# Optimization experiments

Hardware: AMD Instinct MI355X
Metric: run time of the kernel (lower is better)

## Reference

```python
import jax, jax.numpy as jnp
import numpy as np

NHEAD = 3
NPTS = 5
HID = 96
B_GRAPHS = 16384
COORDS_WEIGHT = 1.0


def _ln(x, g, b):
    mu = jnp.mean(x, -1, keepdims=True)
    v = jnp.mean((x - mu) ** 2, -1, keepdims=True)
    return (x - mu) / jnp.sqrt(v + 1e-5) * g + b


def _build_edge_index():
    # fully-connected per graph, grouped by source node (row-major over sources)
    idx = np.arange(NPTS)
    src = np.repeat(idx, NPTS - 1)
    dst = np.concatenate([np.delete(idx, i) for i in range(NPTS)])
    off = (np.arange(B_GRAPHS) * NPTS)[:, None]
    row = (off + src[None, :]).reshape(-1)
    col = (off + dst[None, :]).reshape(-1)
    return jnp.asarray(np.stack([row, col]), dtype=jnp.int32)


def setup_inputs():
    key = jax.random.key(0)
    ks = jax.random.split(key, 24)
    Nn = B_GRAPHS * NPTS          # 81920 nodes
    E = B_GRAPHS * NPTS * (NPTS - 1)  # 327680 edges

    def w(k, i, o):
        return jax.random.normal(k, (i, o), jnp.float32) * (1.0 / np.sqrt(i))

    inp = {
        'h': jax.random.normal(ks[0], (Nn, HID), jnp.float32),
        'edge_index': _build_edge_index(),
        'coord': jax.random.normal(ks[1], (Nn, 3), jnp.float32),
        'coord_pre': jax.random.normal(ks[2], (Nn, 3), jnp.float32),
        'vel': jax.random.normal(ks[3], (Nn, 3), jnp.float32),
        'edge_attr': jax.random.normal(ks[4], (E, HID), jnp.float32),
        # edge_mlp
        'ew1': w(ks[5], 3 * HID, HID), 'eb1': jnp.zeros((HID,), jnp.float32),
        'ew2': w(ks[6], HID, HID), 'eb2': jnp.zeros((HID,), jnp.float32),
        # edge_mlp_enhance
        'xw1': w(ks[7], 3 * HID, HID), 'xb1': jnp.zeros((HID,), jnp.float32),
        'xw2': w(ks[8], HID, HID), 'xb2': jnp.zeros((HID,), jnp.float32),
        # node_mlp
        'nw1': w(ks[9], 2 * HID, HID), 'nb1': jnp.zeros((HID,), jnp.float32),
        'nw2': w(ks[10], HID, HID), 'nb2': jnp.zeros((HID,), jnp.float32),
        # coord_mlp_inner
        'cw1': w(ks[11], HID, HID), 'cb1': jnp.zeros((HID,), jnp.float32),
        'cw2': w(ks[12], HID, HID), 'cb2': jnp.zeros((HID,), jnp.float32),
        'cw3': w(ks[13], HID, 3), 'cb3': jnp.zeros((3,), jnp.float32),
        # attention projections
        'qw': w(ks[14], HID, HID), 'qb': jnp.zeros((HID,), jnp.float32),
        'kw': w(ks[15], 2 * HID, HID), 'kb': jnp.zeros((HID,), jnp.float32),
        'vw': w(ks[16], HID, HID), 'vb': jnp.zeros((HID,), jnp.float32),
        # layernorms
        'g1': jnp.ones((HID,), jnp.float32), 'be1': jnp.zeros((HID,), jnp.float32),
        'g2': jnp.ones((HID,), jnp.float32), 'be2': jnp.zeros((HID,), jnp.float32),
    }
    return inp


def _forward(h, edge_index, coord, coord_pre, vel, edge_attr,
             ew1, eb1, ew2, eb2, xw1, xb1, xw2, xb2, nw1, nb1, nw2, nb2,
             cw1, cb1, cw2, cb2, cw3, cb3, qw, qb, kw, kb, vw, vb,
             g1, be1, g2, be2):
    sp = jax.nn.softplus
    row, col = edge_index[0], edge_index[1]
    n_nodes = h.shape[0]

    # edge_model (attention flag is False)
    ef = sp(jnp.concatenate([h[row], h[col], edge_attr], 1) @ ew1 + eb1)
    ef = sp(ef @ ew2 + eb2)  # [E, C]

    B, N, C = n_nodes // NPTS, NPTS, ef.shape[-1]
    d = C // NHEAD
    q = h.reshape(B, N, C)
    m = ef.reshape(B, N, N - 1, C)
    h_m = jnp.concatenate(
        [jnp.broadcast_to(q[:, :, None, :], (B, N, N - 1, C)), m], -1
    ).reshape(B, N * (N - 1), 2 * C)

    qh = (q @ qw + qb).reshape(B, N, NHEAD, d).transpose(0, 2, 1, 3)           # [B,H,N,d]
    kh = (h_m @ kw + kb).reshape(B, N * (N - 1), NHEAD, d).transpose(0, 2, 1, 3)
    kh = kh.reshape(B, NHEAD, N, N - 1, d)                                      # [B,H,N,N-1,d]
    vh = (ef.reshape(B, N * (N - 1), C) @ vw + vb).reshape(B, N * (N - 1), NHEAD, d).transpose(0, 2, 1, 3)

    scores = jnp.einsum('bhnd,bhnkd->bhnk', qh, kh) / jnp.sqrt(jnp.float32(d))
    attw = jax.nn.softmax(scores, -1)                                           # [B,H,N,N-1]
    m_update = attw.reshape(B, NHEAD, N * (N - 1), 1) * vh                      # [B,H,E',d]
    att_edge_feat = m_update.transpose(0, 2, 1, 3).reshape(-1, C)               # [E, C]

    # node_model
    agg = jax.ops.segment_sum(att_edge_feat, row, num_segments=n_nodes)
    agg = _ln(agg, g1, be1)
    out = sp(jnp.concatenate([h, agg], 1) @ nw1 + nb1) @ nw2 + nb2
    hn = _ln(h + out, g2, be2)

    # edge enhance
    ef2 = ef + (sp(jnp.concatenate([hn[row], hn[col], edge_attr], 1) @ xw1 + xb1) @ xw2 + xb2)

    # coord2radial on coord_pre (norm_diff=False)
    cd = coord_pre[row] - coord_pre[col]
    cc = jnp.cross(coord_pre[row], coord_pre[col])
    cv = jnp.cross(cd, cc)

    # acc_model_inner
    t = sp(ef2 @ cw1 + cb1)
    t = sp(t @ cw2 + cb2)
    bc = t @ cw3 + cb3                                                          # [E, 3]
    trans = jnp.clip(cd * bc[:, :1] + cc * bc[:, 1:2] + cv * bc[:, 2:3], -100.0, 100.0)
    s = jax.ops.segment_sum(trans, row, num_segments=n_nodes)
    cnt = jax.ops.segment_sum(jnp.ones_like(trans), row, num_segments=n_nodes)
    acc = (s / jnp.maximum(cnt, 1.0)) * COORDS_WEIGHT

    return acc, hn, ef2


def reference(h, edge_index, coord, coord_pre, vel, edge_attr,
              ew1, eb1, ew2, eb2, xw1, xb1, xw2, xb2, nw1, nb1, nw2, nb2,
              cw1, cb1, cw2, cb2, cw3, cb3, qw, qb, kw, kb, vw, vb,
              g1, be1, g2, be2):
    return _forward(h, edge_index, coord, coord_pre, vel, edge_attr,
                    ew1, eb1, ew2, eb2, xw1, xb1, xw2, xb2, nw1, nb1, nw2, nb2,
                    cw1, cb1, cw2, cb2, cw3, cb3, qw, qb, kw, kb, vw, vb,
                    g1, be1, g2, be2)
```

## Files before the change

kernel.cpp:

```cpp
#include <hip/hip_runtime.h>
#include <hip/hip_bf16.h>

#define B_GRAPHS 16384
#define NN (B_GRAPHS * 5)
#define NE (NN * 4)
#define GPB 4
#define EPB 80
#define NPB 20

typedef __attribute__((ext_vector_type(8))) short bf8;
typedef __attribute__((ext_vector_type(4))) short s4;
typedef __attribute__((ext_vector_type(4))) float f4;
typedef __attribute__((ext_vector_type(2))) unsigned u2;
typedef __attribute__((ext_vector_type(4))) unsigned u4;

#define OFF_EW1 0
#define OFF_EW2 27648
#define OFF_KW  36864
#define OFF_VW  55296
#define OFF_QW  64512
#define OFF_NW1 73728
#define OFF_NW2 92160
#define OFF_XW1 101376
#define OFF_XW2 129024
#define OFF_CW1 138240
#define OFF_CW2 147456

__device__ __forceinline__ float sp_f(float x) {
    return fmaxf(x, 0.0f) + __logf(1.0f + __expf(-fabsf(x)));
}
__device__ __forceinline__ short tobf(float x) {
    return __builtin_bit_cast(short, __float2bfloat16(x));
}
__device__ __forceinline__ float frombf(short s) {
    union { float f; unsigned u; } v;
    v.u = ((unsigned)(unsigned short)s) << 16;
    return v.f;
}
__device__ __forceinline__ unsigned pk2(float a, float b) {
    unsigned lo = (unsigned short)tobf(a);
    unsigned hi = (unsigned short)tobf(b);
    return lo | (hi << 16);
}
__device__ __forceinline__ bf8 ldfrag(const short* buf, int row, int k) {
    return *(const bf8*)&buf[(row * 96 + k) ^ ((row & 7) << 3)];
}
__device__ __forceinline__ void stpk(short* buf, int row, int col0, f4 v) {
    u2 o = {pk2(v[0], v[1]), pk2(v[2], v[3])};
    *(u2*)&buf[(row * 96 + col0) ^ ((row & 7) << 3)] = o;
}
__device__ __forceinline__ void stpk8(short* buf, int row, int col0,
                                      const float* v) {
    u4 o = {pk2(v[0], v[1]), pk2(v[2], v[3]), pk2(v[4], v[5]), pk2(v[6], v[7])};
    *(u4*)&buf[(row * 96 + col0) ^ ((row & 7) << 3)] = o;
}
__device__ __forceinline__ float* oaddr(float* b, int row, int col) {
    return &b[(row * 96 + col) ^ ((row & 7) << 2)];
}

template <int K, int NS, class AF>
__device__ __forceinline__ void gemmCol(const short* __restrict__ wT, int wc0,
                                        int ln, int kg, AF aload, f4* acc) {
#pragma unroll
    for (int s = 0; s < NS; s++) {
        acc[s][0] = 0.f; acc[s][1] = 0.f; acc[s][2] = 0.f; acc[s][3] = 0.f;
    }
#pragma unroll
    for (int k0 = 0; k0 < K; k0 += 32) {
        bf8 wf = *(const bf8*)(wT + (size_t)(wc0 + ln) * K + k0 + kg * 8);
#pragma unroll
        for (int s = 0; s < NS; s++) {
            acc[s] = __builtin_amdgcn_mfma_f32_16x16x32_bf16(wf, aload(s, k0),
                                                             acc[s], 0, 0, 0);
        }
    }
}

__global__ __launch_bounds__(256) void k_prep(
    const float* ew1, const float* ew2, const float* kw, const float* vw,
    const float* qw, const float* nw1, const float* nw2, const float* xw1,
    const float* xw2, const float* cw1, const float* cw2, short* wsT) {
    const float* srcs[11] = {ew1, ew2, kw, vw, qw, nw1, nw2, xw1, xw2, cw1, cw2};
    const int Ks[11] = {288, 96, 192, 96, 96, 192, 96, 288, 96, 96, 96};
    const int offs[11] = {OFF_EW1, OFF_EW2, OFF_KW, OFF_VW, OFF_QW, OFF_NW1,
                          OFF_NW2, OFF_XW1, OFF_XW2, OFF_CW1, OFF_CW2};
    int b = blockIdx.x;
    const float* src = srcs[b];
    int K = Ks[b], off = offs[b];
    for (int idx = threadIdx.x; idx < K * 96; idx += 256) {
        int n = idx / K, k = idx - n * K;
        wsT[off + idx] = tobf(src[(size_t)k * 96 + n]);
    }
}

__global__ __launch_bounds__(384, 4) void k_fused(
    const float* __restrict__ h, const float* __restrict__ cp,
    const float* __restrict__ ea, const short* __restrict__ wsT,
    const float* __restrict__ eb1, const float* __restrict__ eb2,
    const float* __restrict__ qb, const float* __restrict__ kb,
    const float* __restrict__ vb, const float* __restrict__ nb1,
    const float* __restrict__ nb2, const float* __restrict__ g1,
    const float* __restrict__ be1, const float* __restrict__ g2,
    const float* __restrict__ be2, const float* __restrict__ xb1,
    const float* __restrict__ xb2, const float* __restrict__ cb1,
    const float* __restrict__ cb2, const float* __restrict__ cw3,
    const float* __restrict__ cb3,
    float* __restrict__ accg, float* __restrict__ hng, float* __restrict__ efg) {
    __shared__ __align__(16) short smem[24960];
    short* hb  = smem;
    short* S1  = smem + 1920;
    short* efb = smem + 9600;
    short* kvb = smem + 17280;
    short* qag = S1 + 48 * 96;
    float* sc   = (float*)S1;
    float* outb = (float*)(S1 + 3072);
    float* cw3e = (float*)efb;
    float* bcb  = (float*)(efb + 576);
    float* trs  = (float*)(efb + 1056);

    const int t = threadIdx.x;
    const int blk = blockIdx.x;
    const int n0 = blk * NPB, e0 = blk * EPB;

    for (int i = t; i < 1920; i += 384) {
        int r = i / 24, c = (i - r * 24) * 4;
        f4 v = *(const f4*)&ea[(size_t)(e0 + r) * 96 + c];
        stpk(kvb, r, c, v);
    }
    for (int i = t; i < 480; i += 384) {
        int r = i / 24, c = (i - r * 24) * 4;
        f4 v = *(const f4*)&h[(size_t)(n0 + r) * 96 + c];
        stpk(hb, r, c, v);
    }
    __syncthreads();

    const int lane = t & 63, w = t >> 6;
    const int kg = lane >> 4, ln = lane & 15;
    const int wc0 = w * 16, col0 = wc0 + kg * 4;

    int erow[5], esrc[5], edst[5];
#pragma unroll
    for (int s = 0; s < 5; s++) {
        erow[s] = s * 16 + ln;
        int sl = erow[s] >> 2;
        esrc[s] = sl;
        int si = sl % 5, jj = erow[s] & 3;
        edst[s] = (sl / 5) * 5 + jj + (jj >= si);
    }

    f4 acc[5];
    gemmCol<288, 5>(wsT + OFF_EW1, wc0, ln, kg,
        [&](int s, int k0) -> bf8 {
            int k = k0 + kg * 8;
            if (k0 < 96)  return ldfrag(hb, esrc[s], k);
            if (k0 < 192) return ldfrag(hb, edst[s], k - 96);
            return ldfrag(kvb, erow[s], k - 192);
        }, acc);
    {
        f4 b = *(const f4*)&eb1[col0];
#pragma unroll
        for (int s = 0; s < 5; s++) {
            f4 v;
#pragma unroll
            for (int j = 0; j < 4; j++) v[j] = sp_f(acc[s][j] + b[j]);
            stpk(S1, erow[s], col0, v);
        }
    }
    __syncthreads();
    gemmCol<96, 5>(wsT + OFF_EW2, wc0, ln, kg,
        [&](int s, int k0) { return ldfrag(S1, erow[s], k0 + kg * 8); }, acc);
    {
        f4 b = *(const f4*)&eb2[col0];
#pragma unroll
        for (int s = 0; s < 5; s++) {
            f4 v;
#pragma unroll
            for (int j = 0; j < 4; j++) v[j] = sp_f(acc[s][j] + b[j]);
            stpk(efb, erow[s], col0, v);
        }
    }
    __syncthreads();
    {
        f4 qa[2];
        gemmCol<96, 2>(wsT + OFF_QW, wc0, ln, kg,
            [&](int s, int k0) { return ldfrag(hb, s * 16 + ln, k0 + kg * 8); }, qa);
        f4 b = *(const f4*)&qb[col0];
#pragma unroll
        for (int s = 0; s < 2; s++) {
            int row = s * 16 + ln;
            if (row < NPB) {
                f4 v;
#pragma unroll
                for (int j = 0; j < 4; j++) v[j] = qa[s][j] + b[j];
                stpk(qag, row, col0, v);
            }
        }
    }
    gemmCol<192, 5>(wsT + OFF_KW, wc0, ln, kg,
        [&](int s, int k0) {
            int k = k0 + kg * 8;
            if (k0 < 96) return ldfrag(hb, esrc[s], k);
            return ldfrag(efb, erow[s], k - 96);
        }, acc);
    {
        f4 b = *(const f4*)&kb[col0];
#pragma unroll
        for (int s = 0; s < 5; s++) {
            f4 v;
#pragma unroll
            for (int j = 0; j < 4; j++) v[j] = acc[s][j] + b[j];
            stpk(kvb, erow[s], col0, v);
        }
    }
    __syncthreads();
    if (t < 240) {
        int e = t / 3, hd = t - e * 3, nd = e >> 2;
        float s = 0.f;
#pragma unroll
        for (int c8 = 0; c8 < 4; c8++) {
            int c = hd * 32 + c8 * 8;
            bf8 qv = ldfrag(qag, nd, c);
            bf8 kv = ldfrag(kvb, e, c);
#pragma unroll
            for (int j = 0; j < 8; j++) s = fmaf(frombf(qv[j]), frombf(kv[j]), s);
        }
        sc[e * 3 + hd] = s * 0.17677669529663687f;
    }
    __syncthreads();
    if (t < 60) {
        int nd = t / 3, hd = t - nd * 3;
        float v0 = sc[(nd * 4 + 0) * 3 + hd], v1 = sc[(nd * 4 + 1) * 3 + hd];
        float v2 = sc[(nd * 4 + 2) * 3 + hd], v3 = sc[(nd * 4 + 3) * 3 + hd];
        float m = fmaxf(fmaxf(v0, v1), fmaxf(v2, v3));
        float p0 = __expf(v0 - m), p1 = __expf(v1 - m);
        float p2 = __expf(v2 - m), p3 = __expf(v3 - m);
        float inv = 1.f / (p0 + p1 + p2 + p3);
        sc[(nd * 4 + 0) * 3 + hd] = p0 * inv;
        sc[(nd * 4 + 1) * 3 + hd] = p1 * inv;
        sc[(nd * 4 + 2) * 3 + hd] = p2 * inv;
        sc[(nd * 4 + 3) * 3 + hd] = p3 * inv;
    }
    gemmCol<96, 5>(wsT + OFF_VW, wc0, ln, kg,
        [&](int s, int k0) { return ldfrag(efb, erow[s], k0 + kg * 8); }, acc);
    {
        f4 b = *(const f4*)&vb[col0];
#pragma unroll
        for (int s = 0; s < 5; s++) {
            f4 v;
#pragma unroll
            for (int j = 0; j < 4; j++) v[j] = acc[s][j] + b[j];
            stpk(kvb, erow[s], col0, v);
        }
    }
    __syncthreads();
    if (t < 320) {
        int nd = t >> 4, cg = t & 15;
        bool act = cg < 12;
        int hd = cg >> 2;
        float agg[8];
#pragma unroll
        for (int j = 0; j < 8; j++) agg[j] = 0.f;
        if (act) {
#pragma unroll
            for (int k = 0; k < 4; k++) {
                int e = nd * 4 + k;
                float wgt = sc[e * 3 + hd];
                bf8 v8 = ldfrag(kvb, e, cg * 8);
#pragma unroll
                for (int j = 0; j < 8; j++) agg[j] = fmaf(wgt, frombf(v8[j]), agg[j]);
            }
        }
        float s1 = 0.f, s2 = 0.f;
#pragma unroll
        for (int j = 0; j < 8; j++) { s1 += agg[j]; s2 += agg[j] * agg[j]; }
        if (!act) { s1 = 0.f; s2 = 0.f; }
        for (int m = 1; m < 16; m <<= 1) {
            s1 += __shfl_xor(s1, m);
            s2 += __shfl_xor(s2, m);
        }
        float mu = s1 * (1.f / 96.f);
        float var = s2 * (1.f / 96.f) - mu * mu;
        float rs = rsqrtf(var + 1e-5f);
        if (act) {
            int c = cg * 8;
            f4 ga = *(const f4*)&g1[c], gb = *(const f4*)&g1[c + 4];
            f4 ba = *(const f4*)&be1[c], bb = *(const f4*)&be1[c + 4];
            float o[8];
#pragma unroll
            for (int j = 0; j < 4; j++) {
                o[j] = (agg[j] - mu) * rs * ga[j] + ba[j];
                o[j + 4] = (agg[j + 4] - mu) * rs * gb[j] + bb[j];
            }
            stpk8(qag, nd, c, o);
        }
    }
    __syncthreads();
    for (int i = t; i < 1920; i += 384) {
        int r = i / 24, c = (i - r * 24) * 4;
        f4 v = *(const f4*)&ea[(size_t)(e0 + r) * 96 + c];
        stpk(kvb, r, c, v);
    }
    {
        f4 na[2];
        gemmCol<192, 2>(wsT + OFF_NW1, wc0, ln, kg,
            [&](int s, int k0) {
                int row = s * 16 + ln, k = k0 + kg * 8;
                if (k0 < 96) return ldfrag(hb, row, k);
                return ldfrag(qag, row, k - 96);
            }, na);
        f4 b = *(const f4*)&nb1[col0];
#pragma unroll
        for (int s = 0; s < 2; s++) {
            int row = s * 16 + ln;
            f4 v;
#pragma unroll
            for (int j = 0; j < 4; j++) v[j] = sp_f(na[s][j] + b[j]);
            stpk(S1, row, col0, v);
        }
    }
    __syncthreads();
    {
        f4 na[2];
        gemmCol<96, 2>(wsT + OFF_NW2, wc0, ln, kg,
            [&](int s, int k0) { return ldfrag(S1, s * 16 + ln, k0 + kg * 8); }, na);
        f4 b = *(const f4*)&nb2[col0];
#pragma unroll
        for (int s = 0; s < 2; s++) {
            int row = s * 16 + ln;
            if (row < NPB) {
                f4 hv = *(const f4*)&h[(size_t)(n0 + row) * 96 + col0];
                f4 v;
#pragma unroll
                for (int j = 0; j < 4; j++) v[j] = na[s][j] + b[j] + hv[j];
                *(f4*)oaddr(outb, row, col0) = v;
            }
        }
    }
    __syncthreads();
    if (t < 320) {
        int nd = t >> 4, cg = t & 15;
        bool act = cg < 12;
        float xv[8];
#pragma unroll
        for (int j = 0; j < 8; j++) xv[j] = 0.f;
        if (act) {
            f4 x0 = *(const f4*)oaddr(outb, nd, cg * 8);
            f4 x1 = *(const f4*)oaddr(outb, nd, cg * 8 + 4);
#pragma unroll
            for (int j = 0; j < 4; j++) { xv[j] = x0[j]; xv[j + 4] = x1[j]; }
        }
        float s1 = 0.f, s2 = 0.f;
#pragma unroll
        for (int j = 0; j < 8; j++) { s1 += xv[j]; s2 += xv[j] * xv[j]; }
        for (int m = 1; m < 16; m <<= 1) {
            s1 += __shfl_xor(s1, m);
            s2 += __shfl_xor(s2, m);
        }
        float mu = s1 * (1.f / 96.f);
        float var = s2 * (1.f / 96.f) - mu * mu;
        float rs = rsqrtf(var + 1e-5f);
        if (act) {
            int c = cg * 8;
            f4 ga = *(const f4*)&g2[c], gb = *(const f4*)&g2[c + 4];
            f4 ba = *(const f4*)&be2[c], bb = *(const f4*)&be2[c + 4];
            float o[8];
#pragma unroll
            for (int j = 0; j < 4; j++) {
                o[j] = (xv[j] - mu) * rs * ga[j] + ba[j];
                o[j + 4] = (xv[j + 4] - mu) * rs * gb[j] + bb[j];
            }
            f4 o0 = {o[0], o[1], o[2], o[3]}, o1 = {o[4], o[5], o[6], o[7]};
            *(f4*)&hng[(size_t)(n0 + nd) * 96 + c] = o0;
            *(f4*)&hng[(size_t)(n0 + nd) * 96 + c + 4] = o1;
            stpk8(hb, nd, c, o);
        }
    }
    __syncthreads();
    gemmCol<288, 5>(wsT + OFF_XW1, wc0, ln, kg,
        [&](int s, int k0) -> bf8 {
            int k = k0 + kg * 8;
            if (k0 < 96)  return ldfrag(hb, esrc[s], k);
            if (k0 < 192) return ldfrag(hb, edst[s], k - 96);
            return ldfrag(kvb, erow[s], k - 192);
        }, acc);
    {
        f4 b = *(const f4*)&xb1[col0];
#pragma unroll
        for (int s = 0; s < 5; s++) {
            f4 v;
#pragma unroll
            for (int j = 0; j < 4; j++) v[j] = sp_f(acc[s][j] + b[j]);
            stpk(S1, erow[s], col0, v);
        }
    }
    __syncthreads();
    gemmCol<96, 5>(wsT + OFF_XW2, wc0, ln, kg,
        [&](int s, int k0) { return ldfrag(S1, erow[s], k0 + kg * 8); }, acc);
    {
        f4 b = *(const f4*)&xb2[col0];
#pragma unroll
        for (int s = 0; s < 5; s++) {
            int row = erow[s];
            s4 ev = *(const s4*)&efb[(row * 96 + col0) ^ ((row & 7) << 3)];
            f4 v;
#pragma unroll
            for (int j = 0; j < 4; j++) v[j] = acc[s][j] + b[j] + frombf(ev[j]);
            *(f4*)&efg[(size_t)(e0 + row) * 96 + col0] = v;
            stpk(efb, row, col0, v);
        }
    }
    __syncthreads();
    gemmCol<96, 5>(wsT + OFF_CW1, wc0, ln, kg,
        [&](int s, int k0) { return ldfrag(efb, erow[s], k0 + kg * 8); }, acc);
    {
        f4 b = *(const f4*)&cb1[col0];
#pragma unroll
        for (int s = 0; s < 5; s++) {
            f4 v;
#pragma unroll
            for (int j = 0; j < 4; j++) v[j] = sp_f(acc[s][j] + b[j]);
            stpk(S1, erow[s], col0, v);
        }
    }
    __syncthreads();
    if (t < 288) cw3e[t] = cw3[t];
    gemmCol<96, 5>(wsT + OFF_CW2, wc0, ln, kg,
        [&](int s, int k0) { return ldfrag(S1, erow[s], k0 + kg * 8); }, acc);
    {
        f4 b = *(const f4*)&cb2[col0];
#pragma unroll
        for (int s = 0; s < 5; s++) {
            f4 v;
#pragma unroll
            for (int j = 0; j < 4; j++) v[j] = sp_f(acc[s][j] + b[j]);
            stpk(kvb, erow[s], col0, v);
        }
    }
    __syncthreads();
    if (t < 240) {
        int e = t / 3, j = t - e * 3;
        float s = cb3[j];
#pragma unroll
        for (int c8 = 0; c8 < 12; c8++) {
            bf8 av = ldfrag(kvb, e, c8 * 8);
#pragma unroll
            for (int jj = 0; jj < 8; jj++)
                s = fmaf(frombf(av[jj]), cw3e[(c8 * 8 + jj) * 3 + j], s);
        }
        bcb[e * 3 + j] = s;
    }
    __syncthreads();
    if (t < 80) {
        int sl = t >> 2, jj = t & 3, si = sl % 5;
        int dl = (sl / 5) * 5 + jj + (jj >= si);
        int rn = n0 + sl, cn = n0 + dl;
        float r0c = cp[(size_t)rn * 3 + 0], r1c = cp[(size_t)rn * 3 + 1],
              r2c = cp[(size_t)rn * 3 + 2];
        float q0 = cp[(size_t)cn * 3 + 0], q1 = cp[(size_t)cn * 3 + 1],
              q2 = cp[(size_t)cn * 3 + 2];
        float d0 = r0c - q0, d1 = r1c - q1, d2 = r2c - q2;
        float x0 = r1c * q2 - r2c * q1;
        float x1 = r2c * q0 - r0c * q2;
        float x2 = r0c * q1 - r1c * q0;
        float v0 = d1 * x2 - d2 * x1;
        float v1 = d2 * x0 - d0 * x2;
        float v2 = d0 * x1 - d1 * x0;
        float b0 = bcb[t * 3 + 0], b1 = bcb[t * 3 + 1], b2 = bcb[t * 3 + 2];
        trs[t * 4 + 0] = fminf(fmaxf(d0 * b0 + x0 * b1 + v0 * b2, -100.f), 100.f);
        trs[t * 4 + 1] = fminf(fmaxf(d1 * b0 + x1 * b1 + v1 * b2, -100.f), 100.f);
        trs[t * 4 + 2] = fminf(fmaxf(d2 * b0 + x2 * b1 + v2 * b2, -100.f), 100.f);
    }
    __syncthreads();
    if (t < 60) {
        int nd = t / 3, j = t - nd * 3;
        float s = (trs[(nd * 4 + 0) * 4 + j] + trs[(nd * 4 + 1) * 4 + j] +
                   trs[(nd * 4 + 2) * 4 + j] + trs[(nd * 4 + 3) * 4 + j]) * 0.25f;
        accg[(size_t)(n0 + nd) * 3 + j] = s;
    }
}

extern "C" void kernel_launch(void* const* d_in, const int* in_sizes, int n_in,
                              void* d_out, int out_size, void* d_ws, size_t ws_size,
                              hipStream_t stream) {
    const float* h   = (const float*)d_in[0];
    const float* cp  = (const float*)d_in[3];
    const float* ea  = (const float*)d_in[5];
    const float* ew1 = (const float*)d_in[6];
    const float* eb1 = (const float*)d_in[7];
    const float* ew2 = (const float*)d_in[8];
    const float* eb2 = (const float*)d_in[9];
    const float* xw1 = (const float*)d_in[10];
    const float* xb1 = (const float*)d_in[11];
    const float* xw2 = (const float*)d_in[12];
    const float* xb2 = (const float*)d_in[13];
    const float* nw1 = (const float*)d_in[14];
    const float* nb1 = (const float*)d_in[15];
    const float* nw2 = (const float*)d_in[16];
    const float* nb2 = (const float*)d_in[17];
    const float* cw1 = (const float*)d_in[18];
    const float* cb1 = (const float*)d_in[19];
    const float* cw2 = (const float*)d_in[20];
    const float* cb2 = (const float*)d_in[21];
    const float* cw3 = (const float*)d_in[22];
    const float* cb3 = (const float*)d_in[23];
    const float* qw  = (const float*)d_in[24];
    const float* qb  = (const float*)d_in[25];
    const float* kw  = (const float*)d_in[26];
    const float* kb  = (const float*)d_in[27];
    const float* vw  = (const float*)d_in[28];
    const float* vb  = (const float*)d_in[29];
    const float* g1  = (const float*)d_in[30];
    const float* be1 = (const float*)d_in[31];
    const float* g2  = (const float*)d_in[32];
    const float* be2 = (const float*)d_in[33];

    float* out  = (float*)d_out;
    float* accg = out;
    float* hng  = out + (size_t)NN * 3;
    float* efg  = out + (size_t)NN * 3 + (size_t)NN * 96;
    short* wsT = (short*)d_ws;

    k_prep<<<11, 256, 0, stream>>>(ew1, ew2, kw, vw, qw, nw1, nw2, xw1, xw2,
                                   cw1, cw2, wsT);
    k_fused<<<B_GRAPHS / GPB, 384, 0, stream>>>(
        h, cp, ea, wsT, eb1, eb2, qb, kb, vb, nb1, nb2, g1, be1, g2, be2,
        xb1, xb2, cb1, cb2, cw3, cb3, accg, hng, efg);
}
```

Before: 355.8 us.

## Replace XOR-swizzled LDS layout with padded rows and restructure buffer reuse

Switches shared-memory tiles from an XOR swizzle on a 96-wide row to a padded 104-element row stride, using precomputed row base offsets to avoid conflicts with simpler address math. Buffers are reassigned so the edge-MLP second layer overlaps the Q projection with one fewer barrier. The edge-attribute reload is issued into registers before the node-MLP GEMM so its latency overlaps compute. Weight fragments are preloaded up front in each GEMM. The node-output buffer now holds bf16 instead of fp32, which changes LayerNorm input precision. More registers and an extra barrier before XW1's epilogue may reduce occupancy.

```diff
diff --git a/kernel.cpp b/kernel.cpp
--- a/kernel.cpp
+++ b/kernel.cpp
@@ -7,6 +7,7 @@
 #define GPB 4
 #define EPB 80
 #define NPB 20
+#define RS 104
 
 typedef __attribute__((ext_vector_type(8))) short bf8;
 typedef __attribute__((ext_vector_type(4))) short s4;
@@ -42,35 +43,36 @@
     unsigned hi = (unsigned short)tobf(b);
     return lo | (hi << 16);
 }
-__device__ __forceinline__ bf8 ldfrag(const short* buf, int row, int k) {
-    return *(const bf8*)&buf[(row * 96 + k) ^ ((row & 7) << 3)];
-}
-__device__ __forceinline__ void stpk(short* buf, int row, int col0, f4 v) {
+__device__ __forceinline__ bf8 ldL(const short* buf, int off) {
+    return *(const bf8*)&buf[off];
+}
+__device__ __forceinline__ void stL(short* buf, int off, f4 v) {
     u2 o = {pk2(v[0], v[1]), pk2(v[2], v[3])};
-    *(u2*)&buf[(row * 96 + col0) ^ ((row & 7) << 3)] = o;
-}
-__device__ __forceinline__ void stpk8(short* buf, int row, int col0,
-                                      const float* v) {
+    *(u2*)&buf[off] = o;
+}
+__device__ __forceinline__ void stL8(short* buf, int off, const float* v) {
     u4 o = {pk2(v[0], v[1]), pk2(v[2], v[3]), pk2(v[4], v[5]), pk2(v[6], v[7])};
-    *(u4*)&buf[(row * 96 + col0) ^ ((row & 7) << 3)] = o;
-}
-__device__ __forceinline__ float* oaddr(float* b, int row, int col) {
-    return &b[(row * 96 + col) ^ ((row & 7) << 2)];
+    *(u4*)&buf[off] = o;
 }
 
 template <int K, int NS, class AF>
 __device__ __forceinline__ void gemmCol(const short* __restrict__ wT, int wc0,
                                         int ln, int kg, AF aload, f4* acc) {
+    constexpr int NK = K / 32;
+    bf8 wf[NK];
+    const short* wp = wT + (size_t)(wc0 + ln) * K + kg * 8;
+#pragma unroll
+    for (int kk = 0; kk < NK; kk++) wf[kk] = *(const bf8*)(wp + kk * 32);
 #pragma unroll
     for (int s = 0; s < NS; s++) {
         acc[s][0] = 0.f; acc[s][1] = 0.f; acc[s][2] = 0.f; acc[s][3] = 0.f;
     }
 #pragma unroll
-    for (int k0 = 0; k0 < K; k0 += 32) {
-        bf8 wf = *(const bf8*)(wT + (size_t)(wc0 + ln) * K + k0 + kg * 8);
+    for (int kk = 0; kk < NK; kk++) {
 #pragma unroll
         for (int s = 0; s < NS; s++) {
-            acc[s] = __builtin_amdgcn_mfma_f32_16x16x32_bf16(wf, aload(s, k0),
+            acc[s] = __builtin_amdgcn_mfma_f32_16x16x32_bf16(wf[kk],
+                                                             aload(s, kk * 32),
                                                              acc[s], 0, 0, 0);
         }
     }
@@ -106,17 +108,15 @@
     const float* __restrict__ cb2, const float* __restrict__ cw3,
     const float* __restrict__ cb3,
     float* __restrict__ accg, float* __restrict__ hng, float* __restrict__ efg) {
-    __shared__ __align__(16) short smem[24960];
-    short* hb  = smem;
-    short* S1  = smem + 1920;
-    short* efb = smem + 9600;
-    short* kvb = smem + 17280;
-    short* qag = S1 + 48 * 96;
-    float* sc   = (float*)S1;
-    float* outb = (float*)(S1 + 3072);
-    float* cw3e = (float*)efb;
-    float* bcb  = (float*)(efb + 576);
-    float* trs  = (float*)(efb + 1056);
+    __shared__ __align__(16) short smem[220 * RS];
+    short* hb = smem;
+    short* SB = smem + 20 * RS;
+    short* E1 = smem + 60 * RS;
+    short* E2 = smem + 140 * RS;
+    float* sc   = (float*)(SB + 20 * RS);
+    float* cw3s = (float*)(SB + 20 * RS);
+    float* bcb  = (float*)(SB + 26 * RS);
+    float* trs  = (float*)(SB + 31 * RS);
 
     const int t = threadIdx.x;
     const int blk = blockIdx.x;
@@ -125,12 +125,12 @@
     for (int i = t; i < 1920; i += 384) {
         int r = i / 24, c = (i - r * 24) * 4;
         f4 v = *(const f4*)&ea[(size_t)(e0 + r) * 96 + c];
-        stpk(kvb, r, c, v);
+        stL(E2, r * RS + c, v);
     }
     for (int i = t; i < 480; i += 384) {
         int r = i / 24, c = (i - r * 24) * 4;
         f4 v = *(const f4*)&h[(size_t)(n0 + r) * 96 + c];
-        stpk(hb, r, c, v);
+        stL(hb, r * RS + c, v);
     }
     __syncthreads();
 
@@ -138,23 +138,25 @@
     const int kg = lane >> 4, ln = lane & 15;
     const int wc0 = w * 16, col0 = wc0 + kg * 4;
 
-    int erow[5], esrc[5], edst[5];
+    int erow[5], ebase[5], sbase[5], dbase[5];
 #pragma unroll
     for (int s = 0; s < 5; s++) {
         erow[s] = s * 16 + ln;
         int sl = erow[s] >> 2;
-        esrc[s] = sl;
         int si = sl % 5, jj = erow[s] & 3;
-        edst[s] = (sl / 5) * 5 + jj + (jj >= si);
+        int dl = (sl / 5) * 5 + jj + (jj >= si);
+        ebase[s] = erow[s] * RS;
+        sbase[s] = sl * RS;
+        dbase[s] = dl * RS;
     }
 
     f4 acc[5];
     gemmCol<288, 5>(wsT + OFF_EW1, wc0, ln, kg,
         [&](int s, int k0) -> bf8 {
             int k = k0 + kg * 8;
-            if (k0 < 96)  return ldfrag(hb, esrc[s], k);
-            if (k0 < 192) return ldfrag(hb, edst[s], k - 96);
-            return ldfrag(kvb, erow[s], k - 192);
+            if (k0 < 96)  return ldL(hb, sbase[s] + k);
+            if (k0 < 192) return ldL(hb, dbase[s] + k - 96);
+            return ldL(E2, ebase[s] + k - 192);
         }, acc);
     {
         f4 b = *(const f4*)&eb1[col0];
@@ -163,44 +165,43 @@
             f4 v;
 #pragma unroll
             for (int j = 0; j < 4; j++) v[j] = sp_f(acc[s][j] + b[j]);
-            stpk(S1, erow[s], col0, v);
+            stL(E1, ebase[s] + col0, v);
         }
     }
     __syncthreads();
     gemmCol<96, 5>(wsT + OFF_EW2, wc0, ln, kg,
-        [&](int s, int k0) { return ldfrag(S1, erow[s], k0 + kg * 8); }, acc);
-    {
-        f4 b = *(const f4*)&eb2[col0];
-#pragma unroll
-        for (int s = 0; s < 5; s++) {
-            f4 v;
-#pragma unroll
-            for (int j = 0; j < 4; j++) v[j] = sp_f(acc[s][j] + b[j]);
-            stpk(efb, erow[s], col0, v);
-        }
-    }
-    __syncthreads();
+        [&](int s, int k0) { return ldL(E1, ebase[s] + k0 + kg * 8); }, acc);
     {
         f4 qa[2];
         gemmCol<96, 2>(wsT + OFF_QW, wc0, ln, kg,
-            [&](int s, int k0) { return ldfrag(hb, s * 16 + ln, k0 + kg * 8); }, qa);
-        f4 b = *(const f4*)&qb[col0];
+            [&](int s, int k0) { return ldL(hb, (s * 16 + ln) * RS + k0 + kg * 8); },
+            qa);
+        f4 b = *(const f4*)&eb2[col0];
+#pragma unroll
+        for (int s = 0; s < 5; s++) {
+            f4 v;
+#pragma unroll
+            for (int j = 0; j < 4; j++) v[j] = sp_f(acc[s][j] + b[j]);
+            stL(E2, ebase[s] + col0, v);
+        }
+        f4 bq = *(const f4*)&qb[col0];
 #pragma unroll
         for (int s = 0; s < 2; s++) {
             int row = s * 16 + ln;
             if (row < NPB) {
                 f4 v;
 #pragma unroll
-                for (int j = 0; j < 4; j++) v[j] = qa[s][j] + b[j];
-                stpk(qag, row, col0, v);
+                for (int j = 0; j < 4; j++) v[j] = qa[s][j] + bq[j];
+                stL(SB, row * RS + col0, v);
             }
         }
     }
+    __syncthreads();
     gemmCol<192, 5>(wsT + OFF_KW, wc0, ln, kg,
         [&](int s, int k0) {
             int k = k0 + kg * 8;
-            if (k0 < 96) return ldfrag(hb, esrc[s], k);
-            return ldfrag(efb, erow[s], k - 96);
+            if (k0 < 96) return ldL(hb, sbase[s] + k);
+            return ldL(E2, ebase[s] + k - 96);
         }, acc);
     {
         f4 b = *(const f4*)&kb[col0];
@@ -209,7 +210,7 @@
             f4 v;
 #pragma unroll
             for (int j = 0; j < 4; j++) v[j] = acc[s][j] + b[j];
-            stpk(kvb, erow[s], col0, v);
+            stL(E1, ebase[s] + col0, v);
         }
     }
     __syncthreads();
@@ -219,8 +220,8 @@
 #pragma unroll
         for (int c8 = 0; c8 < 4; c8++) {
             int c = hd * 32 + c8 * 8;
-            bf8 qv = ldfrag(qag, nd, c);
-            bf8 kv = ldfrag(kvb, e, c);
+            bf8 qv = ldL(SB, nd * RS + c);
+            bf8 kv = ldL(E1, e * RS + c);
 #pragma unroll
             for (int j = 0; j < 8; j++) s = fmaf(frombf(qv[j]), frombf(kv[j]), s);
         }
@@ -241,7 +242,7 @@
         sc[(nd * 4 + 3) * 3 + hd] = p3 * inv;
     }
     gemmCol<96, 5>(wsT + OFF_VW, wc0, ln, kg,
-        [&](int s, int k0) { return ldfrag(efb, erow[s], k0 + kg * 8); }, acc);
+        [&](int s, int k0) { return ldL(E2, ebase[s] + k0 + kg * 8); }, acc);
     {
         f4 b = *(const f4*)&vb[col0];
 #pragma unroll
@@ -249,7 +250,7 @@
             f4 v;
 #pragma unroll
             for (int j = 0; j < 4; j++) v[j] = acc[s][j] + b[j];
-            stpk(kvb, erow[s], col0, v);
+            stL(E1, ebase[s] + col0, v);
         }
     }
     __syncthreads();
@@ -265,7 +266,7 @@
             for (int k = 0; k < 4; k++) {
                 int e = nd * 4 + k;
                 float wgt = sc[e * 3 + hd];
-                bf8 v8 = ldfrag(kvb, e, cg * 8);
+                bf8 v8 = ldL(E1, e * RS + cg * 8);
 #pragma unroll
                 for (int j = 0; j < 8; j++) agg[j] = fmaf(wgt, frombf(v8[j]), agg[j]);
             }
@@ -291,38 +292,47 @@
                 o[j] = (agg[j] - mu) * rs * ga[j] + ba[j];
                 o[j + 4] = (agg[j + 4] - mu) * rs * gb[j] + bb[j];
             }
-            stpk8(qag, nd, c, o);
-        }
-    }
-    __syncthreads();
-    for (int i = t; i < 1920; i += 384) {
-        int r = i / 24, c = (i - r * 24) * 4;
-        f4 v = *(const f4*)&ea[(size_t)(e0 + r) * 96 + c];
-        stpk(kvb, r, c, v);
-    }
-    {
+            stL8(SB, nd * RS + c, o);
+        }
+    }
+    __syncthreads();
+    {
+        f4 eav[5];
+        int rr[5], cc[5];
+#pragma unroll
+        for (int u = 0; u < 5; u++) {
+            int i = t + u * 384;
+            rr[u] = i / 24; cc[u] = (i - rr[u] * 24) * 4;
+            eav[u] = *(const f4*)&ea[(size_t)(e0 + rr[u]) * 96 + cc[u]];
+        }
         f4 na[2];
         gemmCol<192, 2>(wsT + OFF_NW1, wc0, ln, kg,
             [&](int s, int k0) {
                 int row = s * 16 + ln, k = k0 + kg * 8;
-                if (k0 < 96) return ldfrag(hb, row, k);
-                return ldfrag(qag, row, k - 96);
+                if (k0 < 96) return ldL(hb, row * RS + k);
+                return ldL(SB, row * RS + k - 96);
             }, na);
         f4 b = *(const f4*)&nb1[col0];
 #pragma unroll
         for (int s = 0; s < 2; s++) {
             int row = s * 16 + ln;
-            f4 v;
-#pragma unroll
-            for (int j = 0; j < 4; j++) v[j] = sp_f(na[s][j] + b[j]);
-            stpk(S1, row, col0, v);
-        }
+            if (row < NPB) {
+                f4 v;
+#pragma unroll
+                for (int j = 0; j < 4; j++) v[j] = sp_f(na[s][j] + b[j]);
+                stL(SB, (20 + row) * RS + col0, v);
+            }
+        }
+#pragma unroll
+        for (int u = 0; u < 5; u++) stL(E1, rr[u] * RS + cc[u], eav[u]);
     }
     __syncthreads();
     {
         f4 na[2];
         gemmCol<96, 2>(wsT + OFF_NW2, wc0, ln, kg,
-            [&](int s, int k0) { return ldfrag(S1, s * 16 + ln, k0 + kg * 8); }, na);
+            [&](int s, int k0) {
+                return ldL(SB, (20 + s * 16 + ln) * RS + k0 + kg * 8);
+            }, na);
         f4 b = *(const f4*)&nb2[col0];
 #pragma unroll
         for (int s = 0; s < 2; s++) {
@@ -332,7 +342,7 @@
                 f4 v;
 #pragma unroll
                 for (int j = 0; j < 4; j++) v[j] = na[s][j] + b[j] + hv[j];
-                *(f4*)oaddr(outb, row, col0) = v;
+                stL(SB, row * RS + col0, v);
             }
         }
     }
@@ -344,10 +354,9 @@
 #pragma unroll
         for (int j = 0; j < 8; j++) xv[j] = 0.f;
         if (act) {
-            f4 x0 = *(const f4*)oaddr(outb, nd, cg * 8);
-            f4 x1 = *(const f4*)oaddr(outb, nd, cg * 8 + 4);
-#pragma unroll
-            for (int j = 0; j < 4; j++) { xv[j] = x0[j]; xv[j + 4] = x1[j]; }
+            bf8 x = ldL(SB, nd * RS + cg * 8);
+#pragma unroll
+            for (int j = 0; j < 8; j++) xv[j] = frombf(x[j]);
         }
         float s1 = 0.f, s2 = 0.f;
 #pragma unroll
@@ -372,17 +381,18 @@
             f4 o0 = {o[0], o[1], o[2], o[3]}, o1 = {o[4], o[5], o[6], o[7]};
             *(f4*)&hng[(size_t)(n0 + nd) * 96 + c] = o0;
             *(f4*)&hng[(size_t)(n0 + nd) * 96 + c + 4] = o1;
-            stpk8(hb, nd, c, o);
+            stL8(hb, nd * RS + c, o);
         }
     }
     __syncthreads();
     gemmCol<288, 5>(wsT + OFF_XW1, wc0, ln, kg,
         [&](int s, int k0) -> bf8 {
             int k = k0 + kg * 8;
-            if (k0 < 96)  return ldfrag(hb, esrc[s], k);
-            if (k0 < 192) return ldfrag(hb, edst[s], k - 96);
-            return ldfrag(kvb, erow[s], k - 192);
+            if (k0 < 96)  return ldL(hb, sbase[s] + k);
+            if (k0 < 192) return ldL(hb, dbase[s] + k - 96);
+            return ldL(E1, ebase[s] + k - 192);
         }, acc);
+    __syncthreads();
     {
         f4 b = *(const f4*)&xb1[col0];
 #pragma unroll
@@ -390,28 +400,27 @@
             f4 v;
 #pragma unroll
             for (int j = 0; j < 4; j++) v[j] = sp_f(acc[s][j] + b[j]);
-            stpk(S1, erow[s], col0, v);
+            stL(E1, ebase[s] + col0, v);
         }
     }
     __syncthreads();
     gemmCol<96, 5>(wsT + OFF_XW2, wc0, ln, kg,
-        [&](int s, int k0) { return ldfrag(S1, erow[s], k0 + kg * 8); }, acc);
+        [&](int s, int k0) { return ldL(E1, ebase[s] + k0 + kg * 8); }, acc);
     {
         f4 b = *(const f4*)&xb2[col0];
 #pragma unroll
         for (int s = 0; s < 5; s++) {
-            int row = erow[s];
-            s4 ev = *(const s4*)&efb[(row * 96 + col0) ^ ((row & 7) << 3)];
+            s4 ev = *(const s4*)&E2[ebase[s] + col0];
             f4 v;
 #pragma unroll
             for (int j = 0; j < 4; j++) v[j] = acc[s][j] + b[j] + frombf(ev[j]);
-            *(f4*)&efg[(size_t)(e0 + row) * 96 + col0] = v;
-            stpk(efb, row, col0, v);
+            *(f4*)&efg[(size_t)(e0 + erow[s]) * 96 + col0] = v;
+            stL(E2, ebase[s] + col0, v);
         }
     }
     __syncthreads();
     gemmCol<96, 5>(wsT + OFF_CW1, wc0, ln, kg,
-        [&](int s, int k0) { return ldfrag(efb, erow[s], k0 + kg * 8); }, acc);
+        [&](int s, int k0) { return ldL(E2, ebase[s] + k0 + kg * 8); }, acc);
     {
         f4 b = *(const f4*)&cb1[col0];
 #pragma unroll
@@ -419,13 +428,13 @@
             f4 v;
 #pragma unroll
             for (int j = 0; j < 4; j++) v[j] = sp_f(acc[s][j] + b[j]);
-            stpk(S1, erow[s], col0, v);
-        }
-    }
-    __syncthreads();
-    if (t < 288) cw3e[t] = cw3[t];
+            stL(E1, ebase[s] + col0, v);
+        }
+    }
+    __syncthreads();
+    if (t < 288) cw3s[t] = cw3[t];
     gemmCol<96, 5>(wsT + OFF_CW2, wc0, ln, kg,
-        [&](int s, int k0) { return ldfrag(S1, erow[s], k0 + kg * 8); }, acc);
+        [&](int s, int k0) { return ldL(E1, ebase[s] + k0 + kg * 8); }, acc);
     {
         f4 b = *(const f4*)&cb2[col0];
 #pragma unroll
@@ -433,7 +442,7 @@
             f4 v;
 #pragma unroll
             for (int j = 0; j < 4; j++) v[j] = sp_f(acc[s][j] + b[j]);
-            stpk(kvb, erow[s], col0, v);
+            stL(E2, ebase[s] + col0, v);
         }
     }
     __syncthreads();
@@ -442,10 +451,10 @@
         float s = cb3[j];
 #pragma unroll
         for (int c8 = 0; c8 < 12; c8++) {
-            bf8 av = ldfrag(kvb, e, c8 * 8);
+            bf8 av = ldL(E2, e * RS + c8 * 8);
 #pragma unroll
             for (int jj = 0; jj < 8; jj++)
-                s = fmaf(frombf(av[jj]), cw3e[(c8 * 8 + jj) * 3 + j], s);
+                s = fmaf(frombf(av[jj]), cw3s[(c8 * 8 + jj) * 3 + j], s);
         }
         bcb[e * 3 + j] = s;
     }
```

Result: faster. 340.2 us (-4.4%).

## Shrink shared memory buffers and prefetch weight fragments to raise occupancy

Applied to the files above, without the earlier changes.

Reorganizes the LDS buffer plan from four regions (about 50KB) into smaller reused regions (about 39KB) and raises the launch-bounds minimum blocks from 4 to 6, so more workgroups can be resident per CU. It also preloads all weight fragments of each GEMM into registers up front, and prefetches edge_attr into registers during the node MLP GEMM. A bf16 hb buffer replaces the fp32 node-output staging, which changes rounding in the LayerNorm input. Register pressure from the weight preload under the tighter launch bounds may cause spills.

```diff
diff --git a/kernel.cpp b/kernel.cpp
--- a/kernel.cpp
+++ b/kernel.cpp
@@ -54,23 +54,25 @@
     u4 o = {pk2(v[0], v[1]), pk2(v[2], v[3]), pk2(v[4], v[5]), pk2(v[6], v[7])};
     *(u4*)&buf[(row * 96 + col0) ^ ((row & 7) << 3)] = o;
 }
-__device__ __forceinline__ float* oaddr(float* b, int row, int col) {
-    return &b[(row * 96 + col) ^ ((row & 7) << 2)];
-}
 
 template <int K, int NS, class AF>
 __device__ __forceinline__ void gemmCol(const short* __restrict__ wT, int wc0,
                                         int ln, int kg, AF aload, f4* acc) {
+    constexpr int NK = K / 32;
+    bf8 wf[NK];
+    const short* wp = wT + (size_t)(wc0 + ln) * K + kg * 8;
+#pragma unroll
+    for (int kk = 0; kk < NK; kk++) wf[kk] = *(const bf8*)(wp + kk * 32);
 #pragma unroll
     for (int s = 0; s < NS; s++) {
         acc[s][0] = 0.f; acc[s][1] = 0.f; acc[s][2] = 0.f; acc[s][3] = 0.f;
     }
 #pragma unroll
-    for (int k0 = 0; k0 < K; k0 += 32) {
-        bf8 wf = *(const bf8*)(wT + (size_t)(wc0 + ln) * K + k0 + kg * 8);
+    for (int kk = 0; kk < NK; kk++) {
 #pragma unroll
         for (int s = 0; s < NS; s++) {
-            acc[s] = __builtin_amdgcn_mfma_f32_16x16x32_bf16(wf, aload(s, k0),
+            acc[s] = __builtin_amdgcn_mfma_f32_16x16x32_bf16(wf[kk],
+                                                             aload(s, kk * 32),
                                                              acc[s], 0, 0, 0);
         }
     }
@@ -93,7 +95,7 @@
     }
 }
 
-__global__ __launch_bounds__(384, 4) void k_fused(
+__global__ __launch_bounds__(384, 6) void k_fused(
     const float* __restrict__ h, const float* __restrict__ cp,
     const float* __restrict__ ea, const short* __restrict__ wsT,
     const float* __restrict__ eb1, const float* __restrict__ eb2,
@@ -106,17 +108,15 @@
     const float* __restrict__ cb2, const float* __restrict__ cw3,
     const float* __restrict__ cb3,
     float* __restrict__ accg, float* __restrict__ hng, float* __restrict__ efg) {
-    __shared__ __align__(16) short smem[24960];
-    short* hb  = smem;
-    short* S1  = smem + 1920;
-    short* efb = smem + 9600;
-    short* kvb = smem + 17280;
-    short* qag = S1 + 48 * 96;
-    float* sc   = (float*)S1;
-    float* outb = (float*)(S1 + 3072);
-    float* cw3e = (float*)efb;
-    float* bcb  = (float*)(efb + 576);
-    float* trs  = (float*)(efb + 1056);
+    __shared__ __align__(16) short smem[19680];
+    short* hb = smem;
+    short* SB = smem + 1920;
+    short* E1 = smem + 3840;
+    short* E2 = smem + 11520;
+    float* sc   = (float*)(smem + 19200);
+    float* bcb  = sc;
+    float* cw3s = (float*)SB;
+    float* trs  = (float*)(SB + 640);
 
     const int t = threadIdx.x;
     const int blk = blockIdx.x;
@@ -125,7 +125,7 @@
     for (int i = t; i < 1920; i += 384) {
         int r = i / 24, c = (i - r * 24) * 4;
         f4 v = *(const f4*)&ea[(size_t)(e0 + r) * 96 + c];
-        stpk(kvb, r, c, v);
+        stpk(E2, r, c, v);
     }
     for (int i = t; i < 480; i += 384) {
         int r = i / 24, c = (i - r * 24) * 4;
@@ -154,7 +154,7 @@
             int k = k0 + kg * 8;
             if (k0 < 96)  return ldfrag(hb, esrc[s], k);
             if (k0 < 192) return ldfrag(hb, edst[s], k - 96);
-            return ldfrag(kvb, erow[s], k - 192);
+            return ldfrag(E2, erow[s], k - 192);
         }, acc);
     {
         f4 b = *(const f4*)&eb1[col0];
@@ -163,44 +163,42 @@
             f4 v;
 #pragma unroll
             for (int j = 0; j < 4; j++) v[j] = sp_f(acc[s][j] + b[j]);
-            stpk(S1, erow[s], col0, v);
+            stpk(E1, erow[s], col0, v);
         }
     }
     __syncthreads();
     gemmCol<96, 5>(wsT + OFF_EW2, wc0, ln, kg,
-        [&](int s, int k0) { return ldfrag(S1, erow[s], k0 + kg * 8); }, acc);
-    {
-        f4 b = *(const f4*)&eb2[col0];
-#pragma unroll
-        for (int s = 0; s < 5; s++) {
-            f4 v;
-#pragma unroll
-            for (int j = 0; j < 4; j++) v[j] = sp_f(acc[s][j] + b[j]);
-            stpk(efb, erow[s], col0, v);
-        }
-    }
-    __syncthreads();
+        [&](int s, int k0) { return ldfrag(E1, erow[s], k0 + kg * 8); }, acc);
     {
         f4 qa[2];
         gemmCol<96, 2>(wsT + OFF_QW, wc0, ln, kg,
             [&](int s, int k0) { return ldfrag(hb, s * 16 + ln, k0 + kg * 8); }, qa);
-        f4 b = *(const f4*)&qb[col0];
+        f4 b = *(const f4*)&eb2[col0];
+#pragma unroll
+        for (int s = 0; s < 5; s++) {
+            f4 v;
+#pragma unroll
+            for (int j = 0; j < 4; j++) v[j] = sp_f(acc[s][j] + b[j]);
+            stpk(E2, erow[s], col0, v);
+        }
+        f4 bq = *(const f4*)&qb[col0];
 #pragma unroll
         for (int s = 0; s < 2; s++) {
             int row = s * 16 + ln;
             if (row < NPB) {
                 f4 v;
 #pragma unroll
-                for (int j = 0; j < 4; j++) v[j] = qa[s][j] + b[j];
-                stpk(qag, row, col0, v);
+                for (int j = 0; j < 4; j++) v[j] = qa[s][j] + bq[j];
+                stpk(SB, row, col0, v);
             }
         }
     }
+    __syncthreads();
     gemmCol<192, 5>(wsT + OFF_KW, wc0, ln, kg,
         [&](int s, int k0) {
             int k = k0 + kg * 8;
             if (k0 < 96) return ldfrag(hb, esrc[s], k);
-            return ldfrag(efb, erow[s], k - 96);
+            return ldfrag(E2, erow[s], k - 96);
         }, acc);
     {
         f4 b = *(const f4*)&kb[col0];
@@ -209,7 +207,7 @@
             f4 v;
 #pragma unroll
             for (int j = 0; j < 4; j++) v[j] = acc[s][j] + b[j];
-            stpk(kvb, erow[s], col0, v);
+            stpk(E1, erow[s], col0, v);
         }
     }
     __syncthreads();
@@ -219,8 +217,8 @@
 #pragma unroll
         for (int c8 = 0; c8 < 4; c8++) {
             int c = hd * 32 + c8 * 8;
-            bf8 qv = ldfrag(qag, nd, c);
-            bf8 kv = ldfrag(kvb, e, c);
+            bf8 qv = ldfrag(SB, nd, c);
+            bf8 kv = ldfrag(E1, e, c);
 #pragma unroll
             for (int j = 0; j < 8; j++) s = fmaf(frombf(qv[j]), frombf(kv[j]), s);
         }
@@ -241,7 +239,7 @@
         sc[(nd * 4 + 3) * 3 + hd] = p3 * inv;
     }
     gemmCol<96, 5>(wsT + OFF_VW, wc0, ln, kg,
-        [&](int s, int k0) { return ldfrag(efb, erow[s], k0 + kg * 8); }, acc);
+        [&](int s, int k0) { return ldfrag(E2, erow[s], k0 + kg * 8); }, acc);
     {
         f4 b = *(const f4*)&vb[col0];
 #pragma unroll
@@ -249,7 +247,7 @@
             f4 v;
 #pragma unroll
             for (int j = 0; j < 4; j++) v[j] = acc[s][j] + b[j];
-            stpk(kvb, erow[s], col0, v);
+            stpk(E1, erow[s], col0, v);
         }
     }
     __syncthreads();
@@ -265,7 +263,7 @@
             for (int k = 0; k < 4; k++) {
                 int e = nd * 4 + k;
                 float wgt = sc[e * 3 + hd];
-                bf8 v8 = ldfrag(kvb, e, cg * 8);
+                bf8 v8 = ldfrag(E1, e, cg * 8);
 #pragma unroll
                 for (int j = 0; j < 8; j++) agg[j] = fmaf(wgt, frombf(v8[j]), agg[j]);
             }
@@ -291,38 +289,46 @@
                 o[j] = (agg[j] - mu) * rs * ga[j] + ba[j];
                 o[j + 4] = (agg[j + 4] - mu) * rs * gb[j] + bb[j];
             }
-            stpk8(qag, nd, c, o);
-        }
-    }
-    __syncthreads();
-    for (int i = t; i < 1920; i += 384) {
-        int r = i / 24, c = (i - r * 24) * 4;
-        f4 v = *(const f4*)&ea[(size_t)(e0 + r) * 96 + c];
-        stpk(kvb, r, c, v);
-    }
-    {
+            stpk8(SB, nd, c, o);
+        }
+    }
+    __syncthreads();
+    {
+        f4 eav[5];
+        int rr[5], cc[5];
+#pragma unroll
+        for (int u = 0; u < 5; u++) {
+            int i = t + u * 384;
+            rr[u] = i / 24; cc[u] = (i - rr[u] * 24) * 4;
+            eav[u] = *(const f4*)&ea[(size_t)(e0 + rr[u]) * 96 + cc[u]];
+        }
         f4 na[2];
         gemmCol<192, 2>(wsT + OFF_NW1, wc0, ln, kg,
             [&](int s, int k0) {
                 int row = s * 16 + ln, k = k0 + kg * 8;
                 if (k0 < 96) return ldfrag(hb, row, k);
-                return ldfrag(qag, row, k - 96);
+                return ldfrag(SB, row, k - 96);
             }, na);
         f4 b = *(const f4*)&nb1[col0];
+        f4 t1v[2];
+#pragma unroll
+        for (int s = 0; s < 2; s++)
+#pragma unroll
+            for (int j = 0; j < 4; j++) t1v[s][j] = sp_f(na[s][j] + b[j]);
+        __syncthreads();
 #pragma unroll
         for (int s = 0; s < 2; s++) {
             int row = s * 16 + ln;
-            f4 v;
-#pragma unroll
-            for (int j = 0; j < 4; j++) v[j] = sp_f(na[s][j] + b[j]);
-            stpk(S1, row, col0, v);
-        }
+            if (row < NPB) stpk(SB, row, col0, t1v[s]);
+        }
+#pragma unroll
+        for (int u = 0; u < 5; u++) stpk(E1, rr[u], cc[u], eav[u]);
     }
     __syncthreads();
     {
         f4 na[2];
         gemmCol<96, 2>(wsT + OFF_NW2, wc0, ln, kg,
-            [&](int s, int k0) { return ldfrag(S1, s * 16 + ln, k0 + kg * 8); }, na);
+            [&](int s, int k0) { return ldfrag(SB, s * 16 + ln, k0 + kg * 8); }, na);
         f4 b = *(const f4*)&nb2[col0];
 #pragma unroll
         for (int s = 0; s < 2; s++) {
@@ -332,7 +338,7 @@
                 f4 v;
 #pragma unroll
                 for (int j = 0; j < 4; j++) v[j] = na[s][j] + b[j] + hv[j];
-                *(f4*)oaddr(outb, row, col0) = v;
+                stpk(hb, row, col0, v);
             }
         }
     }
@@ -344,10 +350,9 @@
 #pragma unroll
         for (int j = 0; j < 8; j++) xv[j] = 0.f;
         if (act) {
-            f4 x0 = *(const f4*)oaddr(outb, nd, cg * 8);
-            f4 x1 = *(const f4*)oaddr(outb, nd, cg * 8 + 4);
-#pragma unroll
-            for (int j = 0; j < 4; j++) { xv[j] = x0[j]; xv[j + 4] = x1[j]; }
+            bf8 x = ldfrag(hb, nd, cg * 8);
+#pragma unroll
+            for (int j = 0; j < 8; j++) xv[j] = frombf(x[j]);
         }
         float s1 = 0.f, s2 = 0.f;
 #pragma unroll
@@ -381,8 +386,9 @@
             int k = k0 + kg * 8;
             if (k0 < 96)  return ldfrag(hb, esrc[s], k);
             if (k0 < 192) return ldfrag(hb, edst[s], k - 96);
-            return ldfrag(kvb, erow[s], k - 192);
+            return ldfrag(E1, erow[s], k - 192);
         }, acc);
+    __syncthreads();
     {
         f4 b = *(const f4*)&xb1[col0];
 #pragma unroll
@@ -390,28 +396,28 @@
             f4 v;
 #pragma unroll
             for (int j = 0; j < 4; j++) v[j] = sp_f(acc[s][j] + b[j]);
-            stpk(S1, erow[s], col0, v);
+            stpk(E1, erow[s], col0, v);
         }
     }
     __syncthreads();
     gemmCol<96, 5>(wsT + OFF_XW2, wc0, ln, kg,
-        [&](int s, int k0) { return ldfrag(S1, erow[s], k0 + kg * 8); }, acc);
+        [&](int s, int k0) { return ldfrag(E1, erow[s], k0 + kg * 8); }, acc);
     {
         f4 b = *(const f4*)&xb2[col0];
 #pragma unroll
         for (int s = 0; s < 5; s++) {
             int row = erow[s];
-            s4 ev = *(const s4*)&efb[(row * 96 + col0) ^ ((row & 7) << 3)];
+            s4 ev = *(const s4*)&E2[(row * 96 + col0) ^ ((row & 7) << 3)];
             f4 v;
 #pragma unroll
             for (int j = 0; j < 4; j++) v[j] = acc[s][j] + b[j] + frombf(ev[j]);
             *(f4*)&efg[(size_t)(e0 + row) * 96 + col0] = v;
-            stpk(efb, row, col0, v);
+            stpk(E2, row, col0, v);
         }
     }
     __syncthreads();
     gemmCol<96, 5>(wsT + OFF_CW1, wc0, ln, kg,
-        [&](int s, int k0) { return ldfrag(efb, erow[s], k0 + kg * 8); }, acc);
+        [&](int s, int k0) { return ldfrag(E2, erow[s], k0 + kg * 8); }, acc);
     {
         f4 b = *(const f4*)&cb1[col0];
 #pragma unroll
@@ -419,13 +425,13 @@
             f4 v;
 #pragma unroll
             for (int j = 0; j < 4; j++) v[j] = sp_f(acc[s][j] + b[j]);
-            stpk(S1, erow[s], col0, v);
-        }
-    }
-    __syncthreads();
-    if (t < 288) cw3e[t] = cw3[t];
+            stpk(E1, erow[s], col0, v);
+        }
+    }
+    __syncthreads();
+    if (t < 288) cw3s[t] = cw3[t];
     gemmCol<96, 5>(wsT + OFF_CW2, wc0, ln, kg,
-        [&](int s, int k0) { return ldfrag(S1, erow[s], k0 + kg * 8); }, acc);
+        [&](int s, int k0) { return ldfrag(E1, erow[s], k0 + kg * 8); }, acc);
     {
         f4 b = *(const f4*)&cb2[col0];
 #pragma unroll
@@ -433,7 +439,7 @@
             f4 v;
 #pragma unroll
             for (int j = 0; j < 4; j++) v[j] = sp_f(acc[s][j] + b[j]);
-            stpk(kvb, erow[s], col0, v);
+            stpk(E2, erow[s], col0, v);
         }
     }
     __syncthreads();
@@ -442,10 +448,10 @@
         float s = cb3[j];
 #pragma unroll
         for (int c8 = 0; c8 < 12; c8++) {
-            bf8 av = ldfrag(kvb, e, c8 * 8);
+            bf8 av = ldfrag(E2, e, c8 * 8);
 #pragma unroll
             for (int jj = 0; jj < 8; jj++)
-                s = fmaf(frombf(av[jj]), cw3e[(c8 * 8 + jj) * 3 + j], s);
+                s = fmaf(frombf(av[jj]), cw3s[(c8 * 8 + jj) * 3 + j], s);
         }
         bcb[e * 3 + j] = s;
     }
```

Result: slower. 452.2 us (+27.1%).
